# Performance work log

Hardware: AMD Instinct MI355X
Metric: run time of the kernel (lower is better)

Reference implementation:

```python
import jax, jax.numpy as jnp
import numpy as np

DIM = 1536
NUM_HEADS = 16
HEAD_DIM = DIM // NUM_HEADS  # 96
ROPE_DIM = HEAD_DIM // 2     # 48
PT_SEQ = 32
FT_SEQ = 32
EPS = 1e-6


def _rope_tables():
    # VisionRotaryEmbedding(dim=48, pt_seq_len=32): 2D axial rotary tables
    f = 1.0 / (10000.0 ** (np.arange(0, ROPE_DIM, 2, dtype=np.float32)[: ROPE_DIM // 2] / ROPE_DIM))
    pos = np.arange(FT_SEQ, dtype=np.float32) / FT_SEQ * PT_SEQ
    freqs = pos[:, None] * f[None, :]                       # [32, 24]
    freqs = np.repeat(freqs, 2, axis=-1)                    # [32, 48] interleaved
    row = np.broadcast_to(freqs[:, None, :], (FT_SEQ, FT_SEQ, ROPE_DIM))
    col = np.broadcast_to(freqs[None, :, :], (FT_SEQ, FT_SEQ, ROPE_DIM))
    grid = np.concatenate([row, col], axis=-1).reshape(-1, HEAD_DIM)  # [1024, 96]
    return jnp.asarray(np.cos(grid)), jnp.asarray(np.sin(grid))


def _apply_rotary(x, cos, sin):
    # x: [B, S, H, D]; cos/sin: [S, D]; interleaved (use_real_unbind_dim=-1) rotation
    xr = x.reshape(*x.shape[:-1], -1, 2)
    x_rot = jnp.stack([-xr[..., 1], xr[..., 0]], axis=-1).reshape(x.shape)
    return x * cos[None, :, None, :] + x_rot * sin[None, :, None, :]


def _rms_norm(x, w):
    var = jnp.mean(jnp.square(x), axis=-1, keepdims=True)
    return x * jax.lax.rsqrt(var + EPS) * w


def setup_inputs() -> dict:
    key = jax.random.key(0)
    ks = jax.random.split(key, 12)
    s = 1.0 / np.sqrt(DIM)
    return {
        "hidden_states": jax.random.normal(ks[0], (8, 1024, DIM), dtype=jnp.float32),
        "Wq": jax.random.normal(ks[1], (DIM, DIM), dtype=jnp.float32) * s,
        "bq": jax.random.normal(ks[2], (DIM,), dtype=jnp.float32) * 0.01,
        "Wk": jax.random.normal(ks[3], (DIM, DIM), dtype=jnp.float32) * s,
        "bk": jax.random.normal(ks[4], (DIM,), dtype=jnp.float32) * 0.01,
        "Wv": jax.random.normal(ks[5], (DIM, DIM), dtype=jnp.float32) * s,
        "bv": jax.random.normal(ks[6], (DIM,), dtype=jnp.float32) * 0.01,
        "q_norm_w": jnp.ones((HEAD_DIM,), dtype=jnp.float32),
        "k_norm_w": jnp.ones((HEAD_DIM,), dtype=jnp.float32),
        "Wo": jax.random.normal(ks[7], (DIM, DIM), dtype=jnp.float32) * s,
        "bo": jax.random.normal(ks[8], (DIM,), dtype=jnp.float32) * 0.01,
    }


def reference(hidden_states, Wq, bq, Wk, bk, Wv, bv, q_norm_w, k_norm_w, Wo, bo):
    B, S, _ = hidden_states.shape
    cos, sin = _rope_tables()  # [S, HEAD_DIM], constants

    q = hidden_states @ Wq.T + bq
    k = hidden_states @ Wk.T + bk
    v = hidden_states @ Wv.T + bv
    q = q.reshape(B, S, NUM_HEADS, HEAD_DIM)
    k = k.reshape(B, S, NUM_HEADS, HEAD_DIM)
    v = v.reshape(B, S, NUM_HEADS, HEAD_DIM)

    q = _rms_norm(q, q_norm_w)
    k = _rms_norm(k, k_norm_w)
    q = _apply_rotary(q, cos, sin)
    k = _apply_rotary(k, cos, sin)

    scale = 1.0 / np.sqrt(HEAD_DIM)
    scores = jnp.einsum("bshd,bthd->bhst", q, k) * scale  # [B, H, S, S]
    probs = jax.nn.softmax(scores, axis=-1)
    out = jnp.einsum("bhst,bthd->bshd", probs, v)          # [B, S, H, D]
    out = out.reshape(B, S, DIM)
    return out @ Wo.T + bo
```

## Files before the change

kernel.cpp:

```cpp
#include <hip/hip_runtime.h>
#include <hip/hip_bf16.h>
#include <math.h>

typedef __hip_bfloat16 bf16;
typedef __attribute__((ext_vector_type(8))) short short8;
typedef __attribute__((ext_vector_type(4))) short short4v;
typedef __attribute__((ext_vector_type(4))) float f32x4;

#define MFMA16(a, b, c) __builtin_amdgcn_mfma_f32_16x16x32_bf16((a), (b), (c), 0, 0, 0)

typedef const __attribute__((address_space(1))) void GVOID;
typedef __attribute__((address_space(3))) void LVOID;

__device__ __forceinline__ float b2f(short s) {
    union { unsigned u; float f; } v;
    v.u = ((unsigned)(unsigned short)s) << 16;
    return v.f;
}
__device__ __forceinline__ short f2b(float f) {
    union { float f; unsigned u; } v;
    v.f = f;
    unsigned r = v.u + 0x7fffu + ((v.u >> 16) & 1u);
    return (short)(r >> 16);
}
__device__ __forceinline__ unsigned packbf(float a, float b) {
    return ((unsigned)(unsigned short)f2b(a)) | (((unsigned)(unsigned short)f2b(b)) << 16);
}

__global__ void sniff_kernel(const unsigned* __restrict__ X, int* __restrict__ flag) {
    __shared__ int cnt;
    if (threadIdx.x == 0) cnt = 0;
    __syncthreads();
    int c = 0;
    for (int i = threadIdx.x; i < 256; i += 64) {
        unsigned w = X[i];
        unsigned e = (w >> 7) & 0xFFu;
        c += (e > 140u) ? 1 : 0;
    }
    atomicAdd(&cnt, c);
    __syncthreads();
    if (threadIdx.x == 0) *flag = (cnt >= 16) ? 1 : 0;
}

__device__ __forceinline__ void canon8(const void* src, short* dst, int i, int f) {
    short8 o;
    if (f) {
        const float* s = (const float*)src + (size_t)i * 8;
#pragma unroll
        for (int j = 0; j < 8; ++j) o[j] = f2b(s[j]);
    } else {
        o = ((const short8*)src)[i];
    }
    ((short8*)dst)[i] = o;
}

__global__ __launch_bounds__(256) void canon_x_kernel(
    const void* __restrict__ src, short* __restrict__ dst, int n8,
    const int* __restrict__ flag)
{
    int i = blockIdx.x * 256 + threadIdx.x;
    if (i >= n8) return;
    canon8(src, dst, i, *flag);
}

__global__ __launch_bounds__(256) void canon_w4_kernel(
    const void* __restrict__ s0, const void* __restrict__ s1,
    const void* __restrict__ s2, const void* __restrict__ s3,
    short* __restrict__ d0, short* __restrict__ d1,
    short* __restrict__ d2, short* __restrict__ d3,
    const int* __restrict__ flag)
{
    const int m = blockIdx.y;
    const void* src = (m == 0) ? s0 : (m == 1) ? s1 : (m == 2) ? s2 : s3;
    short* dst = (m == 0) ? d0 : (m == 1) ? d1 : (m == 2) ? d2 : d3;
    int i = blockIdx.x * 256 + threadIdx.x;
    canon8(src, dst, i, *flag);
}

__global__ void canon_vec_kernel(
    const void* __restrict__ bq, const void* __restrict__ bk,
    const void* __restrict__ bv, const void* __restrict__ bo,
    const void* __restrict__ qw, const void* __restrict__ kw,
    float* __restrict__ biasqkv, float* __restrict__ boc,
    float* __restrict__ qwc, float* __restrict__ kwc,
    const int* __restrict__ flag)
{
    const int f = *flag;
    for (int i = threadIdx.x; i < 6336; i += 256) {
        const void* src; float* dst; int j;
        if (i < 4608) {
            int m = i / 1536; j = i - m * 1536;
            src = (m == 0) ? bq : (m == 1) ? bk : bv; dst = biasqkv + i;
        } else if (i < 6144) { j = i - 4608; src = bo; dst = boc + j; }
        else if (i < 6240)   { j = i - 6144; src = qw; dst = qwc + j; }
        else                 { j = i - 6240; src = kw; dst = kwc + j; }
        *dst = f ? ((const float*)src)[j] : b2f(((const short*)src)[j]);
    }
}

__global__ void rope_tables_kernel(float* __restrict__ cosT, float* __restrict__ sinT) {
    int idx = blockIdx.x * 256 + threadIdx.x;
    if (idx >= 1024 * 96) return;
    int p = idx / 96;
    int d = idx - p * 96;
    int r = p >> 5, c = p & 31;
    int inRow = (d < 48);
    int dd = inRow ? d : d - 48;
    float pos = inRow ? (float)r : (float)c;
    float ex = -(float)(dd & ~1) / 48.0f;
    float f = powf(10000.0f, ex);
    float ang = pos * f;
    cosT[idx] = cosf(ang);
    sinT[idx] = sinf(ang);
}

__global__ __launch_bounds__(512) void gemm256_kernel(
    const bf16* __restrict__ A, const bf16* __restrict__ Bw,
    const float* __restrict__ bias,
    bf16* __restrict__ O0, bf16* __restrict__ O1, bf16* __restrict__ O2,
    int K, const int* __restrict__ outFlag)
{
    __shared__ __align__(16) short As[2][256 * 64];
    __shared__ __align__(16) short Bs[2][256 * 64];

    const int tid = threadIdx.x;
    const int lane = tid & 63, w = tid >> 6;
    const int wm = w >> 2, wn = w & 3;
    const int li = lane & 15, lg = lane >> 4;

    const int total = gridDim.x * gridDim.y;
    const int pp = blockIdx.y * gridDim.x + blockIdx.x;
    const int lb = (pp & 7) * (total >> 3) + (pp >> 3);
    const int nb = lb % gridDim.x;
    const int mb = lb / gridDim.x;
    const long mBase = (long)mb * 256;
    const long nGlob = (long)nb * 256;

    const bf16* aSrc[4]; const bf16* bSrc[4]; int ldsOff[4];
#pragma unroll
    for (int u = 0; u < 4; ++u) {
        const int L = u * 8192 + tid * 16;
        const int S = L ^ (((L >> 7) & 7) << 4);
        const int srow = S >> 7;
        const int scol = (S & 127) >> 1;
        aSrc[u] = A + (mBase + srow) * K + scol;
        bSrc[u] = Bw + (nGlob + srow) * K + scol;
        ldsOff[u] = L >> 1;
    }
    const int rxor = (li & 7) << 4;
    int kidx[2];
#pragma unroll
    for (int ks = 0; ks < 2; ++ks)
        kidx[ks] = ((ks * 64 + lg * 16) ^ rxor) >> 1;

    f32x4 acc[8][4] = {};
    const int NT = K >> 6;

    auto stage = [&](int tt, int bb) {
        const long kc = (long)tt * 64;
#pragma unroll
        for (int u = 0; u < 4; ++u)
            __builtin_amdgcn_global_load_lds((GVOID*)(aSrc[u] + kc),
                                             (LVOID*)&As[bb][ldsOff[u]], 16, 0, 0);
#pragma unroll
        for (int u = 0; u < 4; ++u)
            __builtin_amdgcn_global_load_lds((GVOID*)(bSrc[u] + kc),
                                             (LVOID*)&Bs[bb][ldsOff[u]], 16, 0, 0);
    };

    stage(0, 0);
    asm volatile("s_waitcnt vmcnt(0)" ::: "memory");
    __builtin_amdgcn_s_barrier();
    asm volatile("" ::: "memory");

    for (int t = 0; t < NT; ++t) {
        const int cb = t & 1;
        if (t + 1 < NT) stage(t + 1, cb ^ 1);
        const short* Ab = &As[cb][0];
        const short* Bb = &Bs[cb][0];
        short8 fa[4][2], fb[2][2];
#pragma unroll
        for (int ph = 0; ph < 4; ++ph) {
            const int qm = ph >> 1, qn = ph & 1;
            if (qn == 0) {
#pragma unroll
                for (int m = 0; m < 4; ++m) {
                    const int row = wm * 128 + (qm * 4 + m) * 16 + li;
#pragma unroll
                    for (int ks = 0; ks < 2; ++ks)
                        fa[m][ks] = *(const short8*)(Ab + row * 64 + kidx[ks]);
                }
            }
#pragma unroll
            for (int n = 0; n < 2; ++n) {
                const int row = wn * 64 + (qn * 2 + n) * 16 + li;
#pragma unroll
                for (int ks = 0; ks < 2; ++ks)
                    fb[n][ks] = *(const short8*)(Bb + row * 64 + kidx[ks]);
            }
            __builtin_amdgcn_sched_barrier(0);
            __builtin_amdgcn_s_setprio(1);
#pragma unroll
            for (int m = 0; m < 4; ++m)
#pragma unroll
                for (int n = 0; n < 2; ++n)
#pragma unroll
                    for (int ks = 0; ks < 2; ++ks)
                        acc[qm * 4 + m][qn * 2 + n] =
                            MFMA16(fa[m][ks], fb[n][ks], acc[qm * 4 + m][qn * 2 + n]);
            __builtin_amdgcn_s_setprio(0);
            __builtin_amdgcn_sched_barrier(0);
            if (ph == 2)
                asm volatile("s_waitcnt vmcnt(0)" ::: "memory");
        }
        __builtin_amdgcn_s_barrier();
        asm volatile("" ::: "memory");
    }

    const int f32out = outFlag ? *outFlag : 0;
    const int mat = nb / 6;
    const long colBase = nGlob - (long)mat * 1536;
    bf16* Ob = (mat == 0) ? O0 : (mat == 1) ? O1 : O2;
    if (f32out) {
        float* Cf = (float*)Ob;
#pragma unroll
        for (int n = 0; n < 4; ++n) {
            const long col = colBase + wn * 64 + n * 16 + li;
            const float bv = bias[nGlob + wn * 64 + n * 16 + li];
#pragma unroll
            for (int m = 0; m < 8; ++m) {
                const long row = mBase + wm * 128 + m * 16 + lg * 4;
#pragma unroll
                for (int i = 0; i < 4; ++i)
                    Cf[(row + i) * 1536 + col] = acc[m][n][i] + bv;
            }
        }
    } else {
#pragma unroll
        for (int n = 0; n < 4; ++n) {
            const long col = colBase + wn * 64 + n * 16 + li;
            const float bv = bias[nGlob + wn * 64 + n * 16 + li];
#pragma unroll
            for (int m = 0; m < 8; ++m) {
                const long row = mBase + wm * 128 + m * 16 + lg * 4;
#pragma unroll
                for (int i = 0; i < 4; ++i)
                    Ob[(row + i) * 1536 + col] = __float2bfloat16(acc[m][n][i] + bv);
            }
        }
    }
}

__global__ __launch_bounds__(256) void gemm128_kernel(
    const bf16* __restrict__ A, const bf16* __restrict__ Bw,
    const float* __restrict__ bias, void* __restrict__ C,
    int K, const int* __restrict__ outFlag)
{
    __shared__ __align__(16) short As[2][128 * 64];
    __shared__ __align__(16) short Bs[2][128 * 64];

    const int tid = threadIdx.x;
    const int lane = tid & 63, w = tid >> 6;
    const int wr = w >> 1, wc = w & 1;
    const int li = lane & 15, lg = lane >> 4;

    const int total = gridDim.x * gridDim.y;
    const int pp = blockIdx.y * gridDim.x + blockIdx.x;
    const int lb = (pp & 7) * (total >> 3) + (pp >> 3);
    const int nb = lb % gridDim.x;
    const int mb = lb / gridDim.x;
    const long mBase = (long)mb * 128;
    const long nBase = (long)nb * 128;

    const bf16* aSrc[4]; const bf16* bSrc[4]; int ldsOff[4];
#pragma unroll
    for (int u = 0; u < 4; ++u) {
        const int L = u * 4096 + tid * 16;
        const int S = L ^ (((L >> 7) & 7) << 4);
        const int srow = S >> 7;
        const int scol = (S & 127) >> 1;
        aSrc[u] = A + (mBase + srow) * K + scol;
        bSrc[u] = Bw + (nBase + srow) * K + scol;
        ldsOff[u] = L >> 1;
    }
    const int rxor = (li & 7) << 4;
    int kidx[2];
#pragma unroll
    for (int ks = 0; ks < 2; ++ks)
        kidx[ks] = ((ks * 64 + lg * 16) ^ rxor) >> 1;

    f32x4 acc[4][4] = {};
    const int NT = K >> 6;

    auto stage = [&](int tt, int bb) {
        const long kc = (long)tt * 64;
#pragma unroll
        for (int u = 0; u < 4; ++u)
            __builtin_amdgcn_global_load_lds((GVOID*)(aSrc[u] + kc),
                                             (LVOID*)&As[bb][ldsOff[u]], 16, 0, 0);
#pragma unroll
        for (int u = 0; u < 4; ++u)
            __builtin_amdgcn_global_load_lds((GVOID*)(bSrc[u] + kc),
                                             (LVOID*)&Bs[bb][ldsOff[u]], 16, 0, 0);
    };

    stage(0, 0);
    asm volatile("s_waitcnt vmcnt(0)" ::: "memory");
    __builtin_amdgcn_s_barrier();
    asm volatile("" ::: "memory");

    for (int t = 0; t < NT; ++t) {
        const int cb = t & 1;
        if (t + 1 < NT) stage(t + 1, cb ^ 1);
        const short* Ab = &As[cb][0];
        const short* Bb = &Bs[cb][0];
#pragma unroll
        for (int ks = 0; ks < 2; ++ks) {
            short8 fa[4], fb[4];
#pragma unroll
            for (int m = 0; m < 4; ++m)
                fa[m] = *(const short8*)(Ab + (wr * 64 + m * 16 + li) * 64 + kidx[ks]);
#pragma unroll
            for (int n = 0; n < 4; ++n)
                fb[n] = *(const short8*)(Bb + (wc * 64 + n * 16 + li) * 64 + kidx[ks]);
            __builtin_amdgcn_sched_barrier(0);
            __builtin_amdgcn_s_setprio(1);
#pragma unroll
            for (int m = 0; m < 4; ++m)
#pragma unroll
                for (int n = 0; n < 4; ++n)
                    acc[m][n] = MFMA16(fa[m], fb[n], acc[m][n]);
            __builtin_amdgcn_s_setprio(0);
            __builtin_amdgcn_sched_barrier(0);
        }
        asm volatile("s_waitcnt vmcnt(0)" ::: "memory");
        __builtin_amdgcn_s_barrier();
        asm volatile("" ::: "memory");
    }

    const int f32out = outFlag ? *outFlag : 0;
    if (f32out) {
        float* Cf = (float*)C;
#pragma unroll
        for (int n = 0; n < 4; ++n) {
            const long col = nBase + wc * 64 + n * 16 + li;
            const float bv = bias[col];
#pragma unroll
            for (int m = 0; m < 4; ++m) {
                const long row = mBase + wr * 64 + m * 16 + lg * 4;
#pragma unroll
                for (int i = 0; i < 4; ++i)
                    Cf[(row + i) * 1536 + col] = acc[m][n][i] + bv;
            }
        }
    } else {
        bf16* Cb = (bf16*)C;
#pragma unroll
        for (int n = 0; n < 4; ++n) {
            const long col = nBase + wc * 64 + n * 16 + li;
            const float bv = bias[col];
#pragma unroll
            for (int m = 0; m < 4; ++m) {
                const long row = mBase + wr * 64 + m * 16 + lg * 4;
#pragma unroll
                for (int i = 0; i < 4; ++i)
                    Cb[(row + i) * 1536 + col] = __float2bfloat16(acc[m][n][i] + bv);
            }
        }
    }
}

__global__ __launch_bounds__(256) void norm_rope_kernel(
    bf16* __restrict__ T, const float* __restrict__ wgt,
    const float* __restrict__ cosT, const float* __restrict__ sinT,
    float scale)
{
    const int row = blockIdx.x * 256 + threadIdx.x;
    const int tok = row >> 4;
    const int h = row & 15;
    const int spos = tok & 1023;
    bf16* p = T + (size_t)tok * 1536 + h * 96;

    float x[96];
#pragma unroll
    for (int v = 0; v < 12; ++v) {
        short8 t = *(const short8*)(p + v * 8);
#pragma unroll
        for (int j = 0; j < 8; ++j) x[v * 8 + j] = b2f(t[j]);
    }
    float ss = 0.f;
#pragma unroll
    for (int d = 0; d < 96; ++d) ss += x[d] * x[d];
    const float rn = scale / sqrtf(ss * (1.0f / 96.0f) + 1e-6f);

    const float* cr = cosT + spos * 96;
    const float* sr = sinT + spos * 96;

#pragma unroll
    for (int v = 0; v < 12; ++v) {
        short8 o;
#pragma unroll
        for (int j = 0; j < 8; j += 2) {
            const int d = v * 8 + j;
            const float x0 = x[d] * rn * wgt[d];
            const float x1 = x[d + 1] * rn * wgt[d + 1];
            o[j]     = f2b(x0 * cr[d] - x1 * sr[d]);
            o[j + 1] = f2b(x1 * cr[d + 1] + x0 * sr[d + 1]);
        }
        *(short8*)(p + v * 8) = o;
    }
}

__global__ __launch_bounds__(256) void attn_kernel(
    const bf16* __restrict__ Q, const bf16* __restrict__ K,
    const bf16* __restrict__ V, bf16* __restrict__ O)
{
    __shared__ __align__(16) short Ks[64 * 100];
    __shared__ __align__(16) short Vt[96 * 76];
    __shared__ __align__(16) short Pl[4][32 * 72];

    const int tid = threadIdx.x;
    const int l = tid & 63, w = tid >> 6;
    const int li = l & 15, lg = l >> 4;

    const int p = blockIdx.x;
    const int lb = (p & 7) * 128 + (p >> 3);
    const int qt = lb & 7;
    const int bh = lb >> 3;
    const int b = bh >> 4, h = bh & 15;
    const size_t tokBase = (size_t)b * 1024;

    short8 aq[2][3];
#pragma unroll
    for (int r = 0; r < 2; ++r) {
        const bf16* qp = Q + (tokBase + qt * 128 + w * 32 + r * 16 + li) * 1536 + h * 96;
#pragma unroll
        for (int kk = 0; kk < 3; ++kk)
            aq[r][kk] = *(const short8*)(qp + kk * 32 + lg * 8);
    }

    float m_r[2] = {-1e30f, -1e30f};
    float l_r[2] = {0.f, 0.f};
    f32x4 o[2][6] = {};

    int kr[3], km[3];
#pragma unroll
    for (int u = 0; u < 3; ++u) {
        const int c = tid + 256 * u;
        kr[u] = c / 12;
        km[u] = (c - kr[u] * 12) * 8;
    }
    const int vr = tid >> 2;
    const int vc0 = (tid & 3) * 24;
    short* Plw = &Pl[w][0];

    short8 kreg[3], vreg[3];
#pragma unroll
    for (int u = 0; u < 3; ++u)
        kreg[u] = *(const short8*)(K + (tokBase + kr[u]) * 1536 + h * 96 + km[u]);
    {
        const bf16* vp = V + (tokBase + vr) * 1536 + h * 96 + vc0;
#pragma unroll
        for (int u = 0; u < 3; ++u) vreg[u] = *(const short8*)(vp + u * 8);
    }

    for (int t0 = 0; t0 < 1024; t0 += 64) {
        __syncthreads();
#pragma unroll
        for (int u = 0; u < 3; ++u)
            *(short8*)&Ks[kr[u] * 100 + km[u]] = kreg[u];
#pragma unroll
        for (int u = 0; u < 3; ++u)
#pragma unroll
            for (int j = 0; j < 8; ++j)
                Vt[(vc0 + u * 8 + j) * 76 + vr] = vreg[u][j];
        __syncthreads();

        const int t1 = (t0 + 64 < 1024) ? t0 + 64 : t0;
#pragma unroll
        for (int u = 0; u < 3; ++u)
            kreg[u] = *(const short8*)(K + (tokBase + t1 + kr[u]) * 1536 + h * 96 + km[u]);
        {
            const bf16* vp = V + (tokBase + t1 + vr) * 1536 + h * 96 + vc0;
#pragma unroll
            for (int u = 0; u < 3; ++u) vreg[u] = *(const short8*)(vp + u * 8);
        }

        f32x4 s4[2][4] = {};
#pragma unroll
        for (int kk = 0; kk < 3; ++kk) {
            short8 fk[4];
#pragma unroll
            for (int kn = 0; kn < 4; ++kn)
                fk[kn] = *(const short8*)&Ks[(kn * 16 + li) * 100 + kk * 32 + lg * 8];
#pragma unroll
            for (int r = 0; r < 2; ++r)
#pragma unroll
                for (int kn = 0; kn < 4; ++kn)
                    s4[r][kn] = MFMA16(fk[kn], aq[r][kk], s4[r][kn]);
        }

#pragma unroll
        for (int r = 0; r < 2; ++r) {
            float mk[4];
#pragma unroll
            for (int kn = 0; kn < 4; ++kn)
                mk[kn] = fmaxf(fmaxf(s4[r][kn][0], s4[r][kn][1]),
                               fmaxf(s4[r][kn][2], s4[r][kn][3]));
            float pm = fmaxf(fmaxf(mk[0], mk[1]), fmaxf(mk[2], mk[3]));
            pm = fmaxf(pm, __shfl_xor(pm, 16));
            pm = fmaxf(pm, __shfl_xor(pm, 32));

            float alpha = 1.0f;
            const bool need = (pm > m_r[r] + 8.0f);
            if (need) { alpha = exp2f(m_r[r] - pm); m_r[r] = pm; }
            const float mn = m_r[r];

            float rs = 0.f;
            unsigned pw[8];
#pragma unroll
            for (int kn = 0; kn < 4; ++kn) {
                float p0 = exp2f(s4[r][kn][0] - mn);
                float p1 = exp2f(s4[r][kn][1] - mn);
                float p2 = exp2f(s4[r][kn][2] - mn);
                float p3 = exp2f(s4[r][kn][3] - mn);
                rs += (p0 + p1) + (p2 + p3);
                pw[kn * 2]     = packbf(p0, p1);
                pw[kn * 2 + 1] = packbf(p2, p3);
            }
            rs += __shfl_xor(rs, 16);
            rs += __shfl_xor(rs, 32);
            l_r[r] = l_r[r] * alpha + rs;
            if (need) {
#pragma unroll
                for (int dn = 0; dn < 6; ++dn)
#pragma unroll
                    for (int i = 0; i < 4; ++i) o[r][dn][i] *= alpha;
            }
            unsigned* Pw = (unsigned*)Plw;
            const int rowW = ((r * 16 + li) * 72) >> 1;
#pragma unroll
            for (int kn = 0; kn < 4; ++kn) {
#pragma unroll
                for (int ip = 0; ip < 2; ++ip)
                    Pw[rowW + ((kn * 16 + lg * 4 + ip * 2) >> 1)] = pw[kn * 2 + ip];
            }
        }

#pragma unroll
        for (int kt = 0; kt < 2; ++kt) {
            short8 pa[2];
#pragma unroll
            for (int r = 0; r < 2; ++r)
                pa[r] = *(const short8*)&Plw[(r * 16 + li) * 72 + kt * 32 + lg * 8];
#pragma unroll
            for (int dn = 0; dn < 6; ++dn) {
                short8 fv = *(const short8*)&Vt[(dn * 16 + li) * 76 + kt * 32 + lg * 8];
#pragma unroll
                for (int r = 0; r < 2; ++r)
                    o[r][dn] = MFMA16(fv, pa[r], o[r][dn]);
            }
        }
    }

#pragma unroll
    for (int r = 0; r < 2; ++r) {
        const float inv = 1.0f / l_r[r];
        const size_t row = tokBase + qt * 128 + w * 32 + r * 16 + li;
#pragma unroll
        for (int dn = 0; dn < 6; ++dn) {
            short4v ov;
#pragma unroll
            for (int i = 0; i < 4; ++i) ov[i] = f2b(o[r][dn][i] * inv);
            *(short4v*)&O[row * 1536 + h * 96 + dn * 16 + lg * 4] = ov;
        }
    }
}

extern "C" void kernel_launch(void* const* d_in, const int* in_sizes, int n_in,
                              void* d_out, int out_size, void* d_ws, size_t ws_size,
                              hipStream_t stream) {
    const void* X  = d_in[0];
    const void* Wq = d_in[1];
    const void* bq = d_in[2];
    const void* Wk = d_in[3];
    const void* bk = d_in[4];
    const void* Wv = d_in[5];
    const void* bv = d_in[6];
    const void* qw = d_in[7];
    const void* kw = d_in[8];
    const void* Wo = d_in[9];
    const void* bo = d_in[10];

    char* ws = (char*)d_ws;
    size_t off = 0;
    int* flag = (int*)ws;                      off += 256;
    float* cosT = (float*)(ws + off);          off += 1024 * 96 * 4;
    float* sinT = (float*)(ws + off);          off += 1024 * 96 * 4;
    float* biasqkv = (float*)(ws + off);       off += 4608 * 4;
    float* boc  = (float*)(ws + off);          off += 1536 * 4;
    float* qwc  = (float*)(ws + off);          off += 128 * 4;
    float* kwc  = (float*)(ws + off);          off += 128 * 4;
    off = (off + 255) & ~(size_t)255;
    bf16* Wc  = (bf16*)(ws + off);             off += (size_t)4608 * 1536 * 2;
    bf16* Woc = (bf16*)(ws + off);             off += (size_t)1536 * 1536 * 2;
    bf16* Xc  = (bf16*)(ws + off);             off += (size_t)8192 * 1536 * 2;
    bf16* Qb  = (bf16*)(ws + off);             off += (size_t)8192 * 1536 * 2;
    bf16* Kb  = (bf16*)(ws + off);             off += (size_t)8192 * 1536 * 2;
    bf16* Vb  = (bf16*)(ws + off);             off += (size_t)8192 * 1536 * 2;
    bf16* AO  = Xc;

    sniff_kernel<<<1, 64, 0, stream>>>((const unsigned*)X, flag);

    canon_x_kernel<<<6144, 256, 0, stream>>>(X, (short*)Xc, 8192 * 1536 / 8, flag);
    canon_w4_kernel<<<dim3(1152, 4), 256, 0, stream>>>(
        Wq, Wk, Wv, Wo,
        (short*)Wc, (short*)(Wc + (size_t)1536 * 1536), (short*)(Wc + (size_t)2 * 1536 * 1536),
        (short*)Woc, flag);
    canon_vec_kernel<<<1, 256, 0, stream>>>(bq, bk, bv, bo, qw, kw,
                                            biasqkv, boc, qwc, kwc, flag);
    rope_tables_kernel<<<384, 256, 0, stream>>>(cosT, sinT);

    gemm256_kernel<<<dim3(18, 32), 512, 0, stream>>>(
        Xc, Wc, biasqkv, Qb, Kb, Vb, 1536, nullptr);

    const float qscale = (float)(0.10206207261596577 * 1.4426950408889634);
    norm_rope_kernel<<<512, 256, 0, stream>>>(Qb, qwc, cosT, sinT, qscale);
    norm_rope_kernel<<<512, 256, 0, stream>>>(Kb, kwc, cosT, sinT, 1.0f);

    attn_kernel<<<1024, 256, 0, stream>>>(Qb, Kb, Vb, AO);

    gemm128_kernel<<<dim3(12, 64), 256, 0, stream>>>(
        AO, Woc, boc, d_out, 1536, flag);
}
```

Before: 441.5 us.

## Restructure QKV GEMM into 8-phase pipelined schedule and rework attention V transpose

```diff
diff --git a/kernel.cpp b/kernel.cpp
--- a/kernel.cpp
+++ b/kernel.cpp
@@ -23,8 +23,16 @@
     unsigned r = v.u + 0x7fffu + ((v.u >> 16) & 1u);
     return (short)(r >> 16);
 }
-__device__ __forceinline__ unsigned packbf(float a, float b) {
-    return ((unsigned)(unsigned short)f2b(a)) | (((unsigned)(unsigned short)f2b(b)) << 16);
+__device__ __forceinline__ unsigned packbf2(float a, float b) {
+    float2 t; t.x = a; t.y = b;
+    __hip_bfloat162 h = __float22bfloat162_rn(t);
+    union { __hip_bfloat162 h; unsigned u; } cv; cv.h = h;
+    return cv.u;
+}
+__device__ __forceinline__ short bf2s(float x) {
+    __hip_bfloat16 h = __float2bfloat16(x);
+    union { __hip_bfloat16 h; short s; } cv; cv.h = h;
+    return cv.s;
 }
 
 __global__ void sniff_kernel(const unsigned* __restrict__ X, int* __restrict__ flag) {
@@ -114,19 +122,21 @@
     sinT[idx] = sinf(ang);
 }
 
-__global__ __launch_bounds__(512) void gemm256_kernel(
+__global__ __launch_bounds__(512, 2) void gemm8p_kernel(
     const bf16* __restrict__ A, const bf16* __restrict__ Bw,
     const float* __restrict__ bias,
     bf16* __restrict__ O0, bf16* __restrict__ O1, bf16* __restrict__ O2,
     int K, const int* __restrict__ outFlag)
 {
-    __shared__ __align__(16) short As[2][256 * 64];
-    __shared__ __align__(16) short Bs[2][256 * 64];
+    __shared__ __align__(16) short As[2][2][8192];
+    __shared__ __align__(16) short Bs[2][2][8192];
 
     const int tid = threadIdx.x;
     const int lane = tid & 63, w = tid >> 6;
     const int wm = w >> 2, wn = w & 3;
     const int li = lane & 15, lg = lane >> 4;
+    const int hbx = wn >> 1;
+    const int rb0 = (wn & 1) * 64;
 
     const int total = gridDim.x * gridDim.y;
     const int pp = blockIdx.y * gridDim.x + blockIdx.x;
@@ -136,85 +146,104 @@
     const long mBase = (long)mb * 256;
     const long nGlob = (long)nb * 256;
 
-    const bf16* aSrc[4]; const bf16* bSrc[4]; int ldsOff[4];
-#pragma unroll
-    for (int u = 0; u < 4; ++u) {
+    int srowL[2], scolL[2], ldso[2];
+#pragma unroll
+    for (int u = 0; u < 2; ++u) {
         const int L = u * 8192 + tid * 16;
         const int S = L ^ (((L >> 7) & 7) << 4);
-        const int srow = S >> 7;
-        const int scol = (S & 127) >> 1;
-        aSrc[u] = A + (mBase + srow) * K + scol;
-        bSrc[u] = Bw + (nGlob + srow) * K + scol;
-        ldsOff[u] = L >> 1;
+        srowL[u] = S >> 7;
+        scolL[u] = (S & 127) >> 1;
+        ldso[u] = L >> 1;
     }
     const int rxor = (li & 7) << 4;
-    int kidx[2];
+    int koff[2];
 #pragma unroll
     for (int ks = 0; ks < 2; ++ks)
-        kidx[ks] = ((ks * 64 + lg * 16) ^ rxor) >> 1;
+        koff[ks] = ((ks * 64 + lg * 16) ^ rxor) >> 1;
 
     f32x4 acc[8][4] = {};
     const int NT = K >> 6;
 
-    auto stage = [&](int tt, int bb) {
-        const long kc = (long)tt * 64;
-#pragma unroll
-        for (int u = 0; u < 4; ++u)
-            __builtin_amdgcn_global_load_lds((GVOID*)(aSrc[u] + kc),
-                                             (LVOID*)&As[bb][ldsOff[u]], 16, 0, 0);
-#pragma unroll
-        for (int u = 0; u < 4; ++u)
-            __builtin_amdgcn_global_load_lds((GVOID*)(bSrc[u] + kc),
-                                             (LVOID*)&Bs[bb][ldsOff[u]], 16, 0, 0);
+    auto stageA = [&](int t, int h) {
+        const long kc = (long)t * 64;
+#pragma unroll
+        for (int u = 0; u < 2; ++u)
+            __builtin_amdgcn_global_load_lds(
+                (GVOID*)(A + (mBase + h * 128 + srowL[u]) * K + kc + scolL[u]),
+                (LVOID*)&As[t & 1][h][ldso[u]], 16, 0, 0);
     };
-
-    stage(0, 0);
-    asm volatile("s_waitcnt vmcnt(0)" ::: "memory");
+    auto stageB = [&](int t, int h) {
+        const long kc = (long)t * 64;
+#pragma unroll
+        for (int u = 0; u < 2; ++u)
+            __builtin_amdgcn_global_load_lds(
+                (GVOID*)(Bw + (nGlob + h * 128 + srowL[u]) * K + kc + scolL[u]),
+                (LVOID*)&Bs[t & 1][h][ldso[u]], 16, 0, 0);
+    };
+
+    short8 fa[4][2], fb[2][2];
+    auto readFA = [&](int buf, int qm) {
+#pragma unroll
+        for (int m = 0; m < 4; ++m) {
+            const int r = qm * 64 + m * 16 + li;
+#pragma unroll
+            for (int ks = 0; ks < 2; ++ks)
+                fa[m][ks] = *(const short8*)&As[buf][wm][r * 64 + koff[ks]];
+        }
+    };
+    auto readFB = [&](int buf, int qn) {
+#pragma unroll
+        for (int n = 0; n < 2; ++n) {
+            const int r = rb0 + qn * 32 + n * 16 + li;
+#pragma unroll
+            for (int ks = 0; ks < 2; ++ks)
+                fb[n][ks] = *(const short8*)&Bs[buf][hbx][r * 64 + koff[ks]];
+        }
+    };
+    auto mfmaPh = [&](int qm, int qn) {
+        __builtin_amdgcn_s_setprio(1);
+#pragma unroll
+        for (int m = 0; m < 4; ++m)
+#pragma unroll
+            for (int n = 0; n < 2; ++n)
+#pragma unroll
+                for (int ks = 0; ks < 2; ++ks)
+                    acc[qm * 4 + m][qn * 2 + n] =
+                        MFMA16(fa[m][ks], fb[n][ks], acc[qm * 4 + m][qn * 2 + n]);
+        __builtin_amdgcn_s_setprio(0);
+    };
+
+#define PH_SYNC1() do { __builtin_amdgcn_s_barrier(); \
+    asm volatile("s_waitcnt lgkmcnt(0)" ::: "memory"); \
+    __builtin_amdgcn_sched_barrier(0); } while (0)
+#define PH_SYNC2() do { __builtin_amdgcn_sched_barrier(0); \
+    __builtin_amdgcn_s_barrier(); } while (0)
+#define PH_SYNC2V() do { __builtin_amdgcn_sched_barrier(0); \
+    asm volatile("s_waitcnt vmcnt(2)" ::: "memory"); \
+    __builtin_amdgcn_s_barrier(); } while (0)
+
+    stageA(0, 0); stageA(0, 1); stageB(0, 0); stageB(0, 1); stageA(1, 0);
+    asm volatile("s_waitcnt vmcnt(2)" ::: "memory");
     __builtin_amdgcn_s_barrier();
-    asm volatile("" ::: "memory");
-
-    for (int t = 0; t < NT; ++t) {
-        const int cb = t & 1;
-        if (t + 1 < NT) stage(t + 1, cb ^ 1);
-        const short* Ab = &As[cb][0];
-        const short* Bb = &Bs[cb][0];
-        short8 fa[4][2], fb[2][2];
-#pragma unroll
-        for (int ph = 0; ph < 4; ++ph) {
-            const int qm = ph >> 1, qn = ph & 1;
-            if (qn == 0) {
-#pragma unroll
-                for (int m = 0; m < 4; ++m) {
-                    const int row = wm * 128 + (qm * 4 + m) * 16 + li;
-#pragma unroll
-                    for (int ks = 0; ks < 2; ++ks)
-                        fa[m][ks] = *(const short8*)(Ab + row * 64 + kidx[ks]);
-                }
-            }
-#pragma unroll
-            for (int n = 0; n < 2; ++n) {
-                const int row = wn * 64 + (qn * 2 + n) * 16 + li;
-#pragma unroll
-                for (int ks = 0; ks < 2; ++ks)
-                    fb[n][ks] = *(const short8*)(Bb + row * 64 + kidx[ks]);
-            }
-            __builtin_amdgcn_sched_barrier(0);
-            __builtin_amdgcn_s_setprio(1);
-#pragma unroll
-            for (int m = 0; m < 4; ++m)
-#pragma unroll
-                for (int n = 0; n < 2; ++n)
-#pragma unroll
-                    for (int ks = 0; ks < 2; ++ks)
-                        acc[qm * 4 + m][qn * 2 + n] =
-                            MFMA16(fa[m][ks], fb[n][ks], acc[qm * 4 + m][qn * 2 + n]);
-            __builtin_amdgcn_s_setprio(0);
-            __builtin_amdgcn_sched_barrier(0);
-            if (ph == 2)
-                asm volatile("s_waitcnt vmcnt(0)" ::: "memory");
-        }
-        __builtin_amdgcn_s_barrier();
-        asm volatile("" ::: "memory");
+
+    for (int j = 0; j < NT / 2; ++j) {
+        const int t1 = 2 * j + 1, t2 = 2 * j + 2, t3 = 2 * j + 3;
+        readFA(0, 0); readFB(0, 0); stageA(t1, 1);
+        PH_SYNC1(); mfmaPh(0, 0); PH_SYNC2();
+        readFB(0, 1); stageB(t1, 0);
+        PH_SYNC1(); mfmaPh(0, 1); PH_SYNC2();
+        readFA(0, 1); readFB(0, 0); stageB(t1, 1);
+        PH_SYNC1(); mfmaPh(1, 0); PH_SYNC2();
+        readFB(0, 1); if (t2 < NT) stageA(t2, 0);
+        PH_SYNC1(); mfmaPh(1, 1); PH_SYNC2V();
+        readFA(1, 0); readFB(1, 0); if (t2 < NT) stageA(t2, 1);
+        PH_SYNC1(); mfmaPh(0, 0); PH_SYNC2();
+        readFB(1, 1); if (t2 < NT) stageB(t2, 0);
+        PH_SYNC1(); mfmaPh(0, 1); PH_SYNC2();
+        readFA(1, 1); readFB(1, 0); if (t2 < NT) stageB(t2, 1);
+        PH_SYNC1(); mfmaPh(1, 0); PH_SYNC2();
+        readFB(1, 1); if (t3 < NT) stageA(t3, 0);
+        PH_SYNC1(); mfmaPh(1, 1); PH_SYNC2V();
     }
 
     const int f32out = outFlag ? *outFlag : 0;
@@ -415,7 +444,7 @@
     const bf16* __restrict__ Q, const bf16* __restrict__ K,
     const bf16* __restrict__ V, bf16* __restrict__ O)
 {
-    __shared__ __align__(16) short Ks[64 * 100];
+    __shared__ __align__(16) short Ks[64 * 104];
     __shared__ __align__(16) short Vt[96 * 76];
     __shared__ __align__(16) short Pl[4][32 * 72];
 
@@ -450,30 +479,39 @@
         kr[u] = c / 12;
         km[u] = (c - kr[u] * 12) * 8;
     }
-    const int vr = tid >> 2;
-    const int vc0 = (tid & 3) * 24;
+    const int t2 = tid >> 3;
+    const int dh = tid & 7;
+    const bf16* vbase = V + (tokBase + 2 * t2) * 1536 + h * 96 + dh * 12;
     short* Plw = &Pl[w][0];
 
-    short8 kreg[3], vreg[3];
+    short8 kreg[3];
+    short4v vr0[3], vr1[3];
 #pragma unroll
     for (int u = 0; u < 3; ++u)
         kreg[u] = *(const short8*)(K + (tokBase + kr[u]) * 1536 + h * 96 + km[u]);
-    {
-        const bf16* vp = V + (tokBase + vr) * 1536 + h * 96 + vc0;
-#pragma unroll
-        for (int u = 0; u < 3; ++u) vreg[u] = *(const short8*)(vp + u * 8);
+#pragma unroll
+    for (int u = 0; u < 3; ++u) {
+        vr0[u] = *(const short4v*)(vbase + u * 4);
+        vr1[u] = *(const short4v*)(vbase + 1536 + u * 4);
     }
 
     for (int t0 = 0; t0 < 1024; t0 += 64) {
         __syncthreads();
 #pragma unroll
         for (int u = 0; u < 3; ++u)
-            *(short8*)&Ks[kr[u] * 100 + km[u]] = kreg[u];
-#pragma unroll
-        for (int u = 0; u < 3; ++u)
-#pragma unroll
-            for (int j = 0; j < 8; ++j)
-                Vt[(vc0 + u * 8 + j) * 76 + vr] = vreg[u][j];
+            *(short8*)&Ks[kr[u] * 104 + km[u]] = kreg[u];
+        {
+            unsigned* Vt32 = (unsigned*)Vt;
+#pragma unroll
+            for (int u = 0; u < 3; ++u)
+#pragma unroll
+                for (int j = 0; j < 4; ++j) {
+                    const int d = dh * 12 + u * 4 + j;
+                    const unsigned pk = ((unsigned)(unsigned short)vr0[u][j]) |
+                                        (((unsigned)(unsigned short)vr1[u][j]) << 16);
+                    Vt32[d * 38 + t2] = pk;
+                }
+        }
         __syncthreads();
 
         const int t1 = (t0 + 64 < 1024) ? t0 + 64 : t0;
@@ -481,9 +519,12 @@
         for (int u = 0; u < 3; ++u)
             kreg[u] = *(const short8*)(K + (tokBase + t1 + kr[u]) * 1536 + h * 96 + km[u]);
         {
-            const bf16* vp = V + (tokBase + t1 + vr) * 1536 + h * 96 + vc0;
-#pragma unroll
-            for (int u = 0; u < 3; ++u) vreg[u] = *(const short8*)(vp + u * 8);
+            const bf16* vp = vbase + (size_t)t1 * 1536;
+#pragma unroll
+            for (int u = 0; u < 3; ++u) {
+                vr0[u] = *(const short4v*)(vp + u * 4);
+                vr1[u] = *(const short4v*)(vp + 1536 + u * 4);
+            }
         }
 
         f32x4 s4[2][4] = {};
@@ -492,7 +533,7 @@
             short8 fk[4];
 #pragma unroll
             for (int kn = 0; kn < 4; ++kn)
-                fk[kn] = *(const short8*)&Ks[(kn * 16 + li) * 100 + kk * 32 + lg * 8];
+                fk[kn] = *(const short8*)&Ks[(kn * 16 + li) * 104 + kk * 32 + lg * 8];
 #pragma unroll
             for (int r = 0; r < 2; ++r)
 #pragma unroll
@@ -525,8 +566,8 @@
                 float p2 = exp2f(s4[r][kn][2] - mn);
                 float p3 = exp2f(s4[r][kn][3] - mn);
                 rs += (p0 + p1) + (p2 + p3);
-                pw[kn * 2]     = packbf(p0, p1);
-                pw[kn * 2 + 1] = packbf(p2, p3);
+                pw[kn * 2]     = packbf2(p0, p1);
+                pw[kn * 2 + 1] = packbf2(p2, p3);
             }
             rs += __shfl_xor(rs, 16);
             rs += __shfl_xor(rs, 32);
@@ -571,7 +612,7 @@
         for (int dn = 0; dn < 6; ++dn) {
             short4v ov;
 #pragma unroll
-            for (int i = 0; i < 4; ++i) ov[i] = f2b(o[r][dn][i] * inv);
+            for (int i = 0; i < 4; ++i) ov[i] = bf2s(o[r][dn][i] * inv);
             *(short4v*)&O[row * 1536 + h * 96 + dn * 16 + lg * 4] = ov;
         }
     }
@@ -621,7 +662,7 @@
                                             biasqkv, boc, qwc, kwc, flag);
     rope_tables_kernel<<<384, 256, 0, stream>>>(cosT, sinT);
 
-    gemm256_kernel<<<dim3(18, 32), 512, 0, stream>>>(
+    gemm8p_kernel<<<dim3(18, 32), 512, 0, stream>>>(
         Xc, Wc, biasqkv, Qb, Kb, Vb, 1536, nullptr);
 
     const float qscale = (float)(0.10206207261596577 * 1.4426950408889634);
```

New measurement: 385.3 us. -12.7%, faster.
